# Performance work log

Measured on AMD Instinct MI355X. Metric: run time of the kernel, lower is better.

## Reference

```python
import jax, jax.numpy as jnp
import numpy as np

B, T, EMB, H = 4, 2048, 1024, 16
S = EMB // H


def setup_inputs() -> dict:
    key = jax.random.key(0)
    ks = jax.random.split(key, 7)
    x = jax.random.normal(ks[0], (B, T, EMB), dtype=jnp.float32)
    pad_amounts = jax.random.randint(ks[1], (B,), 0, 512, dtype=jnp.int64)
    Wk = jax.random.normal(ks[2], (S, S), dtype=jnp.float32) * (1.0 / np.sqrt(S))
    Wq = jax.random.normal(ks[3], (S, S), dtype=jnp.float32) * (1.0 / np.sqrt(S))
    Wv = jax.random.normal(ks[4], (S, S), dtype=jnp.float32) * (1.0 / np.sqrt(S))
    Wu = jax.random.normal(ks[5], (EMB, EMB), dtype=jnp.float32) * (1.0 / np.sqrt(EMB))
    bu = jax.random.normal(ks[6], (EMB,), dtype=jnp.float32) * 0.01
    return {"x": x, "Wk": Wk, "Wq": Wq, "Wv": Wv, "Wu": Wu, "bu": bu,
            "pad_amounts": pad_amounts}


def reference(x, Wk, Wq, Wv, Wu, bu, pad_amounts):
    b, t, e = x.shape
    h = H
    s = e // h
    xh = x.reshape(b, t, h, s)
    # torch Linear: y = x @ W.T (no bias for k/q/v)
    keys = jnp.einsum('bths,os->btho', xh, Wk)
    queries = jnp.einsum('bths,os->btho', xh, Wq)
    values = jnp.einsum('bths,os->btho', xh, Wv)
    # (b,t,h,s) -> (b*h,t,s)
    keys = keys.transpose(0, 2, 1, 3).reshape(b * h, t, s)
    queries = queries.transpose(0, 2, 1, 3).reshape(b * h, t, s)
    values = values.transpose(0, 2, 1, 3).reshape(b * h, t, s)
    scale = e ** 0.25
    queries = queries / scale
    keys = keys / scale
    dot = jnp.einsum('nqs,nks->nqk', queries, keys)  # (b*h, t, t)
    # Faithful to original bug: only the first b flat indices of b*h get masked.
    pad_full = jnp.concatenate([pad_amounts,
                                jnp.zeros(b * h - b, dtype=pad_amounts.dtype)])
    thresh = (t - pad_full)[:, None, None]  # (b*h,1,1); thresh=t -> no mask
    pos = jnp.arange(t)
    mask = (pos[None, :, None] >= thresh) & (pos[None, None, :] >= thresh)
    dot = jnp.where(mask, -jnp.inf, dot)
    att = jax.nn.softmax(dot, axis=2)
    out = jnp.einsum('nqk,nks->nqs', att, values)  # (b*h,t,s)
    out = out.reshape(b, h, t, s).transpose(0, 2, 1, 3).reshape(b, t, h * s)
    return out @ Wu.T + bu
```

## Files before the change

### kernel.cpp

```cpp
#include <hip/hip_runtime.h>


typedef float f32x4 __attribute__((ext_vector_type(4)));
typedef float f32x16 __attribute__((ext_vector_type(16)));
typedef _Float16 f16x2 __attribute__((ext_vector_type(2)));
typedef _Float16 f16x8 __attribute__((ext_vector_type(8)));
typedef unsigned u32x4 __attribute__((ext_vector_type(4)));

#define MFMA16(a, b, c) __builtin_amdgcn_mfma_f32_16x16x32_f16((a), (b), (c), 0, 0, 0)
#define MFMA32(a, b, c) __builtin_amdgcn_mfma_f32_32x32x16_f16((a), (b), (c), 0, 0, 0)

constexpr int Tn = 2048;
constexpr int Bn = 4;
constexpr int EMBn = 1024;
constexpr float NEG_INF = -3.0e38f;

__device__ __forceinline__ float exp2_hw(float x) {
  float r; asm("v_exp_f32 %0, %1" : "=v"(r) : "v"(x)); return r;
}
__device__ __forceinline__ unsigned pkrtz(float lo, float hi) {
  unsigned r; asm("v_cvt_pkrtz_f16_f32 %0, %1, %2" : "=v"(r) : "v"(lo), "v"(hi)); return r;
}
__device__ __forceinline__ unsigned pkadd(unsigned a, unsigned b) {
  unsigned r; asm("v_pk_add_f16 %0, %1, %2" : "=v"(r) : "v"(a), "v"(b)); return r;
}
__device__ __forceinline__ void permswap(unsigned& a, unsigned& b) {
  asm("v_permlane32_swap_b32 %0, %1" : "+v"(a), "+v"(b));
}

__global__ __launch_bounds__(256) void sa_prep(
    const float* __restrict__ Wk, const float* __restrict__ Wq,
    const float* __restrict__ Wv, const float* __restrict__ Wu,
    _Float16* __restrict__ w3, _Float16* __restrict__ wub) {
  int idx = blockIdx.x * 256 + threadIdx.x;
  const float rs = 0.21233046f;
  if (idx < 1048576) wub[idx] = (_Float16)Wu[idx];
  if (idx < 4096) {
    w3[idx]        = (_Float16)(Wk[idx] * rs);
    w3[4096 + idx] = (_Float16)(Wq[idx] * rs);
    w3[8192 + idx] = (_Float16)(Wv[idx]);
  }
}

__global__ __launch_bounds__(256) void sa_qkv(
    const float* __restrict__ x, const _Float16* __restrict__ w3,
    _Float16* __restrict__ Qb, _Float16* __restrict__ Kb, _Float16* __restrict__ Vt) {
  const int wave = threadIdx.x >> 6;
  const int lane = threadIdx.x & 63;
  const int g = lane >> 4, c = lane & 15;
  const int n = blockIdx.y, b = n >> 4, h = n & 15;
  const int t0 = blockIdx.x * 64 + wave * 16;

  f16x8 ax[2];
#pragma unroll
  for (int kk = 0; kk < 2; ++kk) {
    const float* xp = x + ((long)((b * Tn + t0 + c) * 16 + h)) * 64 + kk * 32 + g * 8;
    f32x4 u = *(const f32x4*)xp;
    f32x4 v = *(const f32x4*)(xp + 4);
    f16x8 a;
    a[0] = (_Float16)u[0]; a[1] = (_Float16)u[1]; a[2] = (_Float16)u[2]; a[3] = (_Float16)u[3];
    a[4] = (_Float16)v[0]; a[5] = (_Float16)v[1]; a[6] = (_Float16)v[2]; a[7] = (_Float16)v[3];
    ax[kk] = a;
  }

#pragma unroll
  for (int w = 0; w < 2; ++w) {
    _Float16* dst = w ? Qb : Kb;
#pragma unroll
    for (int ot = 0; ot < 4; ++ot) {
      f32x4 a_ = {0.f, 0.f, 0.f, 0.f};
#pragma unroll
      for (int kk = 0; kk < 2; ++kk) {
        f16x8 wf = *(const f16x8*)(w3 + w * 4096 + (ot * 16 + c) * 64 + kk * 32 + g * 8);
        a_ = MFMA16(ax[kk], wf, a_);
      }
#pragma unroll
      for (int r = 0; r < 4; ++r)
        dst[((long)n * Tn + t0 + g * 4 + r) * 64 + ot * 16 + c] = (_Float16)a_[r];
    }
  }

#pragma unroll
  for (int ot = 0; ot < 4; ++ot) {
    f32x4 a_ = {0.f, 0.f, 0.f, 0.f};
#pragma unroll
    for (int kk = 0; kk < 2; ++kk) {
      f16x8 wf = *(const f16x8*)(w3 + 8192 + (ot * 16 + c) * 64 + kk * 32 + g * 8);
      a_ = MFMA16(wf, ax[kk], a_);
    }
#pragma unroll
    for (int r = 0; r < 4; ++r)
      Vt[((long)n * 64 + ot * 16 + g * 4 + r) * Tn + t0 + c] = (_Float16)a_[r];
  }
}

__global__ __launch_bounds__(256, 4) void sa_flash(
    const _Float16* __restrict__ Qb, const _Float16* __restrict__ Kb,
    const _Float16* __restrict__ Vt, const int* __restrict__ pad32,
    _Float16* __restrict__ AO) {
  const int bid = blockIdx.x;
  const int n = (bid & 7) * 8 + (bid >> 7);
  const int qblk = (bid >> 3) & 15;
  const int tid = threadIdx.x;
  const int wave = tid >> 6;
  const int lane = tid & 63;
  const int ql = lane & 31;
  const int hi = lane >> 5;

  int thresh = Tn;
  if (n < Bn) {
    bool is64 = (pad32[1] == 0 && pad32[3] == 0);
    int pv = is64 ? pad32[2 * n] : pad32[n];
    thresh = Tn - pv;
  }

  const int qbase = qblk * 128 + wave * 32;
  const _Float16* Qh = Qb + (long)n * Tn * 64;
  const _Float16* Kh = Kb + (long)n * Tn * 64;
  const _Float16* Vh = Vt + (long)n * 64 * Tn;

  f16x8 bq[4];
  const _Float16* qp = Qh + (long)(qbase + ql) * 64 + hi * 8;
#pragma unroll
  for (int ks = 0; ks < 4; ++ks) bq[ks] = *(const f16x8*)(qp + ks * 16);

  __shared__ __align__(16) char smem[19456];

  const int kr = tid >> 3, kc = tid & 7;
  const int vs = tid >> 2, vc = tid & 3;
  const _Float16* kgp = Kh + kr * 64 + kc * 8;
  const _Float16* vgp = Vh + (long)vs * Tn + vc * 8;
  char* kw = smem + kr * 144 + kc * 16;
  char* vw = smem + 9216 + vs * 80 + vc * 16;

  const char* krd = smem + ql * 144;
  const char* vrd = smem + 9216 + ql * 80;

  f32x16 o[2];
#pragma unroll
  for (int i = 0; i < 16; ++i) { o[0][i] = 0.f; o[1][i] = 0.f; }
  float l = 0.f;

  const bool qge = (qbase + ql) >= thresh;
  const bool qany = (qbase + 32) > thresh;

  {
    f16x8 k0 = *(const f16x8*)kgp;
    f16x8 v0 = *(const f16x8*)vgp;
    *(f16x8*)kw = k0;
    *(f16x8*)vw = v0;
  }
  __syncthreads();

  int cur = 0;
  for (int kb = 0; kb < Tn; kb += 32) {
    const int kbn = (kb + 32) & (Tn - 1);
    f16x8 kst = *(const f16x8*)(kgp + kbn * 64);
    f16x8 vst = *(const f16x8*)(vgp + kbn);

    const int kbb = cur * 4608;
    const int vbb = cur * 5120;

    f16x8 ka0 = *(const f16x8*)(krd + kbb + 0 + hi * 16);
    f16x8 ka1 = *(const f16x8*)(krd + kbb + 32 + hi * 16);
    f16x8 ka2 = *(const f16x8*)(krd + kbb + 64 + hi * 16);
    f16x8 ka3 = *(const f16x8*)(krd + kbb + 96 + hi * 16);

    f32x16 st;
#pragma unroll
    for (int i = 0; i < 16; ++i) st[i] = 0.f;
    st = MFMA32(ka0, bq[0], st);
    st = MFMA32(ka1, bq[1], st);
    st = MFMA32(ka2, bq[2], st);
    st = MFMA32(ka3, bq[3], st);

    if (qany && (kb + 32) > thresh) {
      if (qge) {
#pragma unroll
        for (int r = 0; r < 16; ++r) {
          int kr_ = kb + (r & 3) + 8 * (r >> 2) + 4 * hi;
          if (kr_ >= thresh) st[r] = NEG_INF;
        }
      }
    }

    float p[16];
#pragma unroll
    for (int r = 0; r < 16; ++r) p[r] = exp2_hw(st[r]);

    unsigned pw[8], psum[2];
#pragma unroll
    for (int j = 0; j < 2; ++j) {
      unsigned a0 = pkrtz(p[j * 8 + 0], p[j * 8 + 1]);
      unsigned b0 = pkrtz(p[j * 8 + 4], p[j * 8 + 5]);
      unsigned a1 = pkrtz(p[j * 8 + 2], p[j * 8 + 3]);
      unsigned b1 = pkrtz(p[j * 8 + 6], p[j * 8 + 7]);
      psum[j] = pkadd(pkadd(a0, b0), pkadd(a1, b1));
      permswap(a0, b0);
      permswap(a1, b1);
      pw[j * 4 + 0] = a0; pw[j * 4 + 1] = a1;
      pw[j * 4 + 2] = b0; pw[j * 4 + 3] = b1;
    }
    {
      f16x2 ph = __builtin_bit_cast(f16x2, pkadd(psum[0], psum[1]));
      l += (float)ph[0] + (float)ph[1];
    }
    u32x4 u0 = {pw[0], pw[1], pw[2], pw[3]};
    u32x4 u1 = {pw[4], pw[5], pw[6], pw[7]};
    f16x8 pb0 = __builtin_bit_cast(f16x8, u0);
    f16x8 pb1 = __builtin_bit_cast(f16x8, u1);

    f16x8 va0 = *(const f16x8*)(vrd + vbb + 0 + hi * 16);
    f16x8 va1 = *(const f16x8*)(vrd + vbb + 32 + hi * 16);
    f16x8 va2 = *(const f16x8*)(vrd + vbb + 2560 + 0 + hi * 16);
    f16x8 va3 = *(const f16x8*)(vrd + vbb + 2560 + 32 + hi * 16);

    o[0] = MFMA32(va0, pb0, o[0]);
    o[0] = MFMA32(va1, pb1, o[0]);
    o[1] = MFMA32(va2, pb0, o[1]);
    o[1] = MFMA32(va3, pb1, o[1]);

    *(f16x8*)(kw + (cur ^ 1) * 4608) = kst;
    *(f16x8*)(vw + (cur ^ 1) * 5120) = vst;
    __syncthreads();
    cur ^= 1;
  }

  float lf = l + __shfl_xor(l, 32, 64);
  float linv = 1.0f / lf;

  _Float16* my = (_Float16*)(smem + wave * 4096);
#pragma unroll
  for (int stile = 0; stile < 2; ++stile) {
#pragma unroll
    for (int r = 0; r < 16; r += 2) {
      unsigned wv = pkrtz(o[stile][r] * linv, o[stile][r + 1] * linv);
      int s = stile * 32 + (r & 3) + 8 * (r >> 2) + 4 * hi;
      *(unsigned*)(my + ql * 64 + (s ^ ((ql & 7) << 3))) = wv;
    }
  }
  asm volatile("s_waitcnt lgkmcnt(0)" ::: "memory");

  const int bb = n >> 4, hh = n & 15;
  const int qr = lane >> 3, s0 = (lane & 7) * 8;
#pragma unroll
  for (int j = 0; j < 4; ++j) {
    int q = j * 8 + qr;
    f16x8 vv = *(const f16x8*)(my + q * 64 + (s0 ^ ((q & 7) << 3)));
    *(f16x8*)(AO + ((long)(bb * Tn + qbase + q)) * EMBn + hh * 64 + s0) = vv;
  }
}

__global__ __launch_bounds__(256, 4) void sa_oproj(
    const _Float16* __restrict__ A, const _Float16* __restrict__ WuB,
    const float* __restrict__ bu, float* __restrict__ Y) {
  const int bid = blockIdx.x;
  const int xcd = bid & 7;
  const int j = bid >> 3;
  const int nstrip = j & 15;
  const int mblk = xcd * 8 + (j >> 4);
  const int tid = threadIdx.x;
  const int wave = tid >> 6;
  const int lane = tid & 63;
  const int ql = lane & 31;
  const int hi = lane >> 5;
  const int mbase = mblk * 128 + wave * 32;
  const int nbase = nstrip * 64;

  __shared__ __align__(16) char bsm[18432];
  const int sr = tid >> 3, sc = tid & 7;
  const _Float16* wg0 = WuB + (long)(nbase + sr) * 1024 + sc * 8;
  const _Float16* wg1 = WuB + (long)(nbase + sr + 32) * 1024 + sc * 8;
  char* ww0 = bsm + sr * 144 + sc * 16;
  char* ww1 = bsm + (sr + 32) * 144 + sc * 16;

  const _Float16* ap = A + (long)(mbase + ql) * 1024 + hi * 8;

  f32x16 acc[2];
#pragma unroll
  for (int i = 0; i < 16; ++i) { acc[0][i] = 0.f; acc[1][i] = 0.f; }

  {
    f16x8 w0 = *(const f16x8*)wg0;
    f16x8 w1 = *(const f16x8*)wg1;
    *(f16x8*)ww0 = w0;
    *(f16x8*)ww1 = w1;
  }
  __syncthreads();

  int cur = 0;
  for (int kb = 0; kb < 1024; kb += 64) {
    const int kbn = (kb + 64) & 1023;
    f16x8 wn0 = *(const f16x8*)(wg0 + kbn);
    f16x8 wn1 = *(const f16x8*)(wg1 + kbn);

    f16x8 af[4];
#pragma unroll
    for (int ks = 0; ks < 4; ++ks) af[ks] = *(const f16x8*)(ap + kb + ks * 16);

    const char* bbase = bsm + cur * 9216;
#pragma unroll
    for (int nt = 0; nt < 2; ++nt) {
      const char* brow = bbase + (nt * 32 + ql) * 144;
#pragma unroll
      for (int ks = 0; ks < 4; ++ks) {
        f16x8 bf = *(const f16x8*)(brow + (ks * 2 + hi) * 16);
        acc[nt] = MFMA32(bf, af[ks], acc[nt]);
      }
    }

    *(f16x8*)(ww0 + (cur ^ 1) * 9216) = wn0;
    *(f16x8*)(ww1 + (cur ^ 1) * 9216) = wn1;
    __syncthreads();
    cur ^= 1;
  }

  float* yrow = Y + (long)(mbase + ql) * 1024;
#pragma unroll
  for (int nt = 0; nt < 2; ++nt) {
#pragma unroll
    for (int qd = 0; qd < 4; ++qd) {
      int nb = nbase + nt * 32 + qd * 8 + 4 * hi;
      f32x4 bv = *(const f32x4*)(bu + nb);
      f32x4 out;
      out[0] = acc[nt][qd * 4 + 0] + bv[0];
      out[1] = acc[nt][qd * 4 + 1] + bv[1];
      out[2] = acc[nt][qd * 4 + 2] + bv[2];
      out[3] = acc[nt][qd * 4 + 3] + bv[3];
      *(f32x4*)(yrow + nb) = out;
    }
  }
}

extern "C" void kernel_launch(void* const* d_in, const int* in_sizes, int n_in,
                              void* d_out, int out_size, void* d_ws, size_t ws_size,
                              hipStream_t stream) {
  const float* x  = (const float*)d_in[0];
  const float* Wk = (const float*)d_in[1];
  const float* Wq = (const float*)d_in[2];
  const float* Wv = (const float*)d_in[3];
  const float* Wu = (const float*)d_in[4];
  const float* bu = (const float*)d_in[5];
  const int* pad  = (const int*)d_in[6];
  float* Y = (float*)d_out;

  _Float16* ws  = (_Float16*)d_ws;
  _Float16* w3  = ws;
  _Float16* wub = ws + 16384;
  _Float16* Qb  = ws + 16384 + 1048576;
  _Float16* Kb  = Qb + 8388608;
  _Float16* Vt  = Kb + 8388608;
  _Float16* AO  = Vt + 8388608;

  sa_prep<<<4096, 256, 0, stream>>>(Wk, Wq, Wv, Wu, w3, wub);
  sa_qkv<<<dim3(32, 64), 256, 0, stream>>>(x, w3, Qb, Kb, Vt);
  sa_flash<<<dim3(1024), 256, 0, stream>>>(Qb, Kb, Vt, pad, AO);
  sa_oproj<<<dim3(1024), 256, 0, stream>>>(AO, wub, bu, Y);
}
```

Measured before the change: 165.4 us.

## Double key tile to 64 per barrier, add MFMA priority hints, transpose output GEMM

The attention loop now stages 64 keys and values per shared-memory buffer and processes them as two 32-key sub-steps, which halves the number of __syncthreads and global-load rounds per key sweep. V is stored row-padded the same way as K. MFMA blocks are wrapped in s_setprio to favour matrix issue across waves. The output projection swaps MFMA operand order so each lane writes a single column with a scalar bias, giving coalesced scalar stores instead of vector row stores. The larger LDS footprint may reduce occupancy.

```diff
diff --git a/kernel.cpp b/kernel.cpp
--- a/kernel.cpp
+++ b/kernel.cpp
@@ -124,21 +124,18 @@
 #pragma unroll
   for (int ks = 0; ks < 4; ++ks) bq[ks] = *(const f16x8*)(qp + ks * 16);
 
-  __shared__ __align__(16) char smem[19456];
-
-  const int kr = tid >> 3, kc = tid & 7;
-  const int vs = tid >> 2, vc = tid & 3;
-  const _Float16* kgp = Kh + kr * 64 + kc * 8;
-  const _Float16* vgp = Vh + (long)vs * Tn + vc * 8;
-  char* kw = smem + kr * 144 + kc * 16;
-  char* vw = smem + 9216 + vs * 80 + vc * 16;
-
-  const char* krd = smem + ql * 144;
-  const char* vrd = smem + 9216 + ql * 80;
+  __shared__ __align__(16) char smem[36864];
+
+  const int sr = tid >> 2, sc = tid & 3;
+  const _Float16* kgp = Kh + sr * 64 + sc * 8;
+  const _Float16* vgp = Vh + (long)sr * Tn + sc * 8;
+  char* kw = smem + sr * 144 + sc * 16;
+  char* vw = smem + 18432 + sr * 144 + sc * 16;
 
   f32x16 o[2];
-#pragma unroll
-  for (int i = 0; i < 16; ++i) { o[0][i] = 0.f; o[1][i] = 0.f; }
+  f32x16 zf;
+#pragma unroll
+  for (int i = 0; i < 16; ++i) { o[0][i] = 0.f; o[1][i] = 0.f; zf[i] = 0.f; }
   float l = 0.f;
 
   const bool qge = (qbase + ql) >= thresh;
@@ -146,82 +143,99 @@
 
   {
     f16x8 k0 = *(const f16x8*)kgp;
+    f16x8 k1 = *(const f16x8*)(kgp + 32);
     f16x8 v0 = *(const f16x8*)vgp;
+    f16x8 v1 = *(const f16x8*)(vgp + 32);
     *(f16x8*)kw = k0;
+    *(f16x8*)(kw + 64) = k1;
     *(f16x8*)vw = v0;
+    *(f16x8*)(vw + 64) = v1;
   }
   __syncthreads();
 
   int cur = 0;
-  for (int kb = 0; kb < Tn; kb += 32) {
-    const int kbn = (kb + 32) & (Tn - 1);
-    f16x8 kst = *(const f16x8*)(kgp + kbn * 64);
-    f16x8 vst = *(const f16x8*)(vgp + kbn);
-
-    const int kbb = cur * 4608;
-    const int vbb = cur * 5120;
-
-    f16x8 ka0 = *(const f16x8*)(krd + kbb + 0 + hi * 16);
-    f16x8 ka1 = *(const f16x8*)(krd + kbb + 32 + hi * 16);
-    f16x8 ka2 = *(const f16x8*)(krd + kbb + 64 + hi * 16);
-    f16x8 ka3 = *(const f16x8*)(krd + kbb + 96 + hi * 16);
-
-    f32x16 st;
-#pragma unroll
-    for (int i = 0; i < 16; ++i) st[i] = 0.f;
-    st = MFMA32(ka0, bq[0], st);
-    st = MFMA32(ka1, bq[1], st);
-    st = MFMA32(ka2, bq[2], st);
-    st = MFMA32(ka3, bq[3], st);
-
-    if (qany && (kb + 32) > thresh) {
-      if (qge) {
-#pragma unroll
-        for (int r = 0; r < 16; ++r) {
-          int kr_ = kb + (r & 3) + 8 * (r >> 2) + 4 * hi;
-          if (kr_ >= thresh) st[r] = NEG_INF;
+  for (int kb = 0; kb < Tn; kb += 64) {
+    const int kbn = (kb + 64) & (Tn - 1);
+    f16x8 kst0 = *(const f16x8*)(kgp + kbn * 64);
+    f16x8 kst1 = *(const f16x8*)(kgp + kbn * 64 + 32);
+    f16x8 vst0 = *(const f16x8*)(vgp + kbn);
+    f16x8 vst1 = *(const f16x8*)(vgp + kbn + 32);
+
+    const char* kbb = smem + cur * 9216;
+    const char* vbb = smem + 18432 + cur * 9216;
+
+#pragma unroll
+    for (int sub = 0; sub < 2; ++sub) {
+      const char* krow = kbb + (sub * 32 + ql) * 144 + hi * 16;
+      f16x8 ka0 = *(const f16x8*)(krow);
+      f16x8 ka1 = *(const f16x8*)(krow + 32);
+      f16x8 ka2 = *(const f16x8*)(krow + 64);
+      f16x8 ka3 = *(const f16x8*)(krow + 96);
+
+      __builtin_amdgcn_s_setprio(1);
+      f32x16 st = MFMA32(ka0, bq[0], zf);
+      st = MFMA32(ka1, bq[1], st);
+      st = MFMA32(ka2, bq[2], st);
+      st = MFMA32(ka3, bq[3], st);
+      __builtin_amdgcn_s_setprio(0);
+
+      if (qany && (kb + sub * 32 + 32) > thresh) {
+        if (qge) {
+#pragma unroll
+          for (int r = 0; r < 16; ++r) {
+            int kr_ = kb + sub * 32 + (r & 3) + 8 * (r >> 2) + 4 * hi;
+            if (kr_ >= thresh) st[r] = NEG_INF;
+          }
         }
       }
-    }
-
-    float p[16];
-#pragma unroll
-    for (int r = 0; r < 16; ++r) p[r] = exp2_hw(st[r]);
-
-    unsigned pw[8], psum[2];
-#pragma unroll
-    for (int j = 0; j < 2; ++j) {
-      unsigned a0 = pkrtz(p[j * 8 + 0], p[j * 8 + 1]);
-      unsigned b0 = pkrtz(p[j * 8 + 4], p[j * 8 + 5]);
-      unsigned a1 = pkrtz(p[j * 8 + 2], p[j * 8 + 3]);
-      unsigned b1 = pkrtz(p[j * 8 + 6], p[j * 8 + 7]);
-      psum[j] = pkadd(pkadd(a0, b0), pkadd(a1, b1));
-      permswap(a0, b0);
-      permswap(a1, b1);
-      pw[j * 4 + 0] = a0; pw[j * 4 + 1] = a1;
-      pw[j * 4 + 2] = b0; pw[j * 4 + 3] = b1;
-    }
-    {
-      f16x2 ph = __builtin_bit_cast(f16x2, pkadd(psum[0], psum[1]));
-      l += (float)ph[0] + (float)ph[1];
-    }
-    u32x4 u0 = {pw[0], pw[1], pw[2], pw[3]};
-    u32x4 u1 = {pw[4], pw[5], pw[6], pw[7]};
-    f16x8 pb0 = __builtin_bit_cast(f16x8, u0);
-    f16x8 pb1 = __builtin_bit_cast(f16x8, u1);
-
-    f16x8 va0 = *(const f16x8*)(vrd + vbb + 0 + hi * 16);
-    f16x8 va1 = *(const f16x8*)(vrd + vbb + 32 + hi * 16);
-    f16x8 va2 = *(const f16x8*)(vrd + vbb + 2560 + 0 + hi * 16);
-    f16x8 va3 = *(const f16x8*)(vrd + vbb + 2560 + 32 + hi * 16);
-
-    o[0] = MFMA32(va0, pb0, o[0]);
-    o[0] = MFMA32(va1, pb1, o[0]);
-    o[1] = MFMA32(va2, pb0, o[1]);
-    o[1] = MFMA32(va3, pb1, o[1]);
-
-    *(f16x8*)(kw + (cur ^ 1) * 4608) = kst;
-    *(f16x8*)(vw + (cur ^ 1) * 5120) = vst;
+
+      float p[16];
+#pragma unroll
+      for (int r = 0; r < 16; ++r) p[r] = exp2_hw(st[r]);
+
+      unsigned pw[8], psum[2];
+#pragma unroll
+      for (int j = 0; j < 2; ++j) {
+        unsigned a0 = pkrtz(p[j * 8 + 0], p[j * 8 + 1]);
+        unsigned b0 = pkrtz(p[j * 8 + 4], p[j * 8 + 5]);
+        unsigned a1 = pkrtz(p[j * 8 + 2], p[j * 8 + 3]);
+        unsigned b1 = pkrtz(p[j * 8 + 6], p[j * 8 + 7]);
+        psum[j] = pkadd(pkadd(a0, b0), pkadd(a1, b1));
+        permswap(a0, b0);
+        permswap(a1, b1);
+        pw[j * 4 + 0] = a0; pw[j * 4 + 1] = a1;
+        pw[j * 4 + 2] = b0; pw[j * 4 + 3] = b1;
+      }
+      {
+        f16x2 ph = __builtin_bit_cast(f16x2, pkadd(psum[0], psum[1]));
+        l += (float)ph[0] + (float)ph[1];
+      }
+      u32x4 u0 = {pw[0], pw[1], pw[2], pw[3]};
+      u32x4 u1 = {pw[4], pw[5], pw[6], pw[7]};
+      f16x8 pb0 = __builtin_bit_cast(f16x8, u0);
+      f16x8 pb1 = __builtin_bit_cast(f16x8, u1);
+
+      const char* vrow0 = vbb + ql * 144 + sub * 64 + hi * 16;
+      const char* vrow1 = vrow0 + 32 * 144;
+      f16x8 va0 = *(const f16x8*)(vrow0);
+      f16x8 va1 = *(const f16x8*)(vrow0 + 32);
+      f16x8 va2 = *(const f16x8*)(vrow1);
+      f16x8 va3 = *(const f16x8*)(vrow1 + 32);
+
+      __builtin_amdgcn_s_setprio(1);
+      o[0] = MFMA32(va0, pb0, o[0]);
+      o[0] = MFMA32(va1, pb1, o[0]);
+      o[1] = MFMA32(va2, pb0, o[1]);
+      o[1] = MFMA32(va3, pb1, o[1]);
+      __builtin_amdgcn_s_setprio(0);
+    }
+
+    char* kwd = kw + (cur ^ 1) * 9216;
+    char* vwd = vw + (cur ^ 1) * 9216;
+    *(f16x8*)kwd = kst0;
+    *(f16x8*)(kwd + 64) = kst1;
+    *(f16x8*)vwd = vst0;
+    *(f16x8*)(vwd + 64) = vst1;
     __syncthreads();
     cur ^= 1;
   }
@@ -305,7 +319,7 @@
 #pragma unroll
       for (int ks = 0; ks < 4; ++ks) {
         f16x8 bf = *(const f16x8*)(brow + (ks * 2 + hi) * 16);
-        acc[nt] = MFMA32(bf, af[ks], acc[nt]);
+        acc[nt] = MFMA32(af[ks], bf, acc[nt]);
       }
     }
 
@@ -315,19 +329,13 @@
     cur ^= 1;
   }
 
-  float* yrow = Y + (long)(mbase + ql) * 1024;
 #pragma unroll
   for (int nt = 0; nt < 2; ++nt) {
-#pragma unroll
-    for (int qd = 0; qd < 4; ++qd) {
-      int nb = nbase + nt * 32 + qd * 8 + 4 * hi;
-      f32x4 bv = *(const f32x4*)(bu + nb);
-      f32x4 out;
-      out[0] = acc[nt][qd * 4 + 0] + bv[0];
-      out[1] = acc[nt][qd * 4 + 1] + bv[1];
-      out[2] = acc[nt][qd * 4 + 2] + bv[2];
-      out[3] = acc[nt][qd * 4 + 3] + bv[3];
-      *(f32x4*)(yrow + nb) = out;
+    float bias = bu[nbase + nt * 32 + ql];
+#pragma unroll
+    for (int r = 0; r < 16; ++r) {
+      int mrow = mbase + (r & 3) + 8 * (r >> 2) + 4 * hi;
+      Y[(long)mrow * 1024 + nbase + nt * 32 + ql] = acc[nt][r] + bias;
     }
   }
 }
```

Measured after the change: 153.0 us. -7.5%, faster.
